# Optimization experiments

Hardware: AMD Instinct MI355X
Metric: run time of the kernel (lower is better)

## Reference

```python
import jax, jax.numpy as jnp
import numpy as np

DIVIDE = 1.0


def setup_inputs() -> dict:
    key = jax.random.key(0)
    ks = jax.random.split(key, 12)
    B, NH, L, H, DIM = 2, 8, 1024, 64, 64
    return {
        "mask": jax.random.normal(ks[0], (B, NH, L, L), dtype=jnp.float32),
        "q": jax.random.normal(ks[1], (B, L, NH, H), dtype=jnp.float32),
        "k": jax.random.normal(ks[2], (B, L, NH, H), dtype=jnp.float32),
        "v": jax.random.normal(ks[3], (B, L, NH, H), dtype=jnp.float32),
        "W0": jax.random.normal(ks[4], (1, DIM), dtype=jnp.float32) * 0.02,
        "b0": jnp.zeros((DIM,), dtype=jnp.float32),
        "W1": jax.random.normal(ks[5], (DIM, DIM), dtype=jnp.float32) * 0.02,
        "b1": jnp.zeros((DIM,), dtype=jnp.float32),
        "W2": jax.random.normal(ks[6], (DIM, DIM), dtype=jnp.float32) * 0.02,
        "b2": jnp.zeros((DIM,), dtype=jnp.float32),
        "Wf": jax.random.normal(ks[7], (DIM, 8), dtype=jnp.float32) * 0.02,
        "bf": jnp.zeros((8,), dtype=jnp.float32),
    }


def reference(mask, q, k, v, W0, b0, W1, b1, W2, b2, Wf, bf):
    # default positions: arange over L1 / L2; identical across batch so we
    # compute the (L1, L2) relative-position grid once and broadcast.
    L1, L2 = q.shape[-3], k.shape[-3]
    pos_q = jnp.arange(L1, dtype=q.dtype)
    pos_k = jnp.arange(L2, dtype=q.dtype)
    rel = (pos_q[:, None] - pos_k[None, :]) / DIVIDE          # (L1, L2)
    rel = rel[..., None]                                       # (L1, L2, 1)
    # depth-3 MLP: Linear -> SiLU (norm=False => Identity), final Linear to n_heads
    h = jax.nn.silu(rel @ W0 + b0)                             # (L1, L2, DIM)
    h = jax.nn.silu(h @ W1 + b1)
    h = jax.nn.silu(h @ W2 + b2)
    bias = h @ Wf + bf                                         # (L1, L2, NH)
    bias = jnp.moveaxis(bias, -1, 0)                           # (NH, L1, L2)
    # mask shapes already match q/k lengths -> no padding branch needed
    return mask - bias                                          # broadcast over B
```

## Files before the change

kernel.cpp:

```cpp
#include <hip/hip_runtime.h>
#include <hip/hip_bf16.h>


#define L_SEQ 1024
#define NDIAG (2 * L_SEQ - 1)
#define NH 8
#define DIM 64

typedef float f32x4 __attribute__((ext_vector_type(4)));

__device__ __forceinline__ float silu_f(float x) {
    return x / (1.0f + __expf(-x));
}

__global__ __launch_bounds__(256) void build_bias_table(
    const float* __restrict__ W0, const float* __restrict__ b0,
    const float* __restrict__ W1, const float* __restrict__ b1,
    const float* __restrict__ W2, const float* __restrict__ b2,
    const float* __restrict__ Wf, const float* __restrict__ bf,
    float* __restrict__ rtab ) {
    const int g = threadIdx.x >> 6;
    const int t = threadIdx.x & 63;
    const int d = blockIdx.x * 4 + g;
    const float rel = (float)(d - (L_SEQ - 1));

    __shared__ float sh[4][DIM];

    float h = silu_f(rel * W0[t] + b0[t]);
    sh[g][t] = h;
    __syncthreads();

    float acc = b1[t];
    #pragma unroll
    for (int k = 0; k < DIM; ++k) acc += sh[g][k] * W1[k * DIM + t];
    float h1 = silu_f(acc);
    __syncthreads();
    sh[g][t] = h1;
    __syncthreads();

    acc = b2[t];
    #pragma unroll
    for (int k = 0; k < DIM; ++k) acc += sh[g][k] * W2[k * DIM + t];
    float h2 = silu_f(acc);
    __syncthreads();
    sh[g][t] = h2;
    __syncthreads();

    if (t < NH && d < NDIAG) {
        float a = bf[t];
        #pragma unroll
        for (int k = 0; k < DIM; ++k) a += sh[g][k] * Wf[k * NH + t];
        rtab[t * NDIAG + (NDIAG - 1 - d)] = a;
    }
}

__global__ __launch_bounds__(256) void apply_bias(
    const f32x4* __restrict__ mask, const float* __restrict__ rtab,
    f32x4* __restrict__ out) {
    const int row = blockIdx.x;
    const int i = row & (L_SEQ - 1);
    const int h = (row >> 10) & (NH - 1);
    const float* rt = rtab + h * NDIAG + (L_SEQ - 1 - i);

    const int t = threadIdx.x;
    const int idx = row * 256 + t;
    const int j0 = t << 2;

    const f32x4 m = mask[idx];
    f32x4 o;
    o.x = m.x - rt[j0 + 0];
    o.y = m.y - rt[j0 + 1];
    o.z = m.z - rt[j0 + 2];
    o.w = m.w - rt[j0 + 3];
    out[idx] = o;
}

extern "C" void kernel_launch(void* const* d_in, const int* in_sizes, int n_in,
                              void* d_out, int out_size, void* d_ws, size_t ws_size,
                              hipStream_t stream) {
    const float* mask = (const float*)d_in[0];
    const float* W0 = (const float*)d_in[4];
    const float* b0 = (const float*)d_in[5];
    const float* W1 = (const float*)d_in[6];
    const float* b1 = (const float*)d_in[7];
    const float* W2 = (const float*)d_in[8];
    const float* b2 = (const float*)d_in[9];
    const float* Wf = (const float*)d_in[10];
    const float* bf = (const float*)d_in[11];
    float* out = (float*)d_out;

    float* rtab = (float*)d_ws;

    build_bias_table<<<(NDIAG + 3) / 4, 256, 0, stream>>>(
        W0, b0, W1, b1, W2, b2, Wf, bf, rtab);

    const int rows = out_size / L_SEQ;
    apply_bias<<<rows, 256, 0, stream>>>(
        (const f32x4*)mask, rtab, (f32x4*)out);
}
```

Baseline: 31.26 us.

## Stage bias diagonal window in LDS and reuse across rows and batches

Each apply_bias block now handles four query rows for one head across both batch elements. It first loads the shared 1027-entry diagonal window of the bias table into padded LDS, then reuses it for eight output rows. This removes the unaligned scalar global gathers of the table per row and cuts table traffic. The cost is more work per block, a sync, fewer blocks (2048), and a hardcoded B=2 grid.

```diff
diff --git a/kernel.cpp b/kernel.cpp
--- a/kernel.cpp
+++ b/kernel.cpp
@@ -54,25 +54,44 @@
     }
 }
 
+__device__ __forceinline__ int SW(int k) { return k + (k >> 5); }
+#define WIN 1027
+#define LDS_FLOATS (WIN + (WIN >> 5) + 1)
+
 __global__ __launch_bounds__(256) void apply_bias(
     const f32x4* __restrict__ mask, const float* __restrict__ rtab,
     f32x4* __restrict__ out) {
-    const int row = blockIdx.x;
-    const int i = row & (L_SEQ - 1);
-    const int h = (row >> 10) & (NH - 1);
-    const float* rt = rtab + h * NDIAG + (L_SEQ - 1 - i);
+    const int blk  = blockIdx.x;
+    const int h    = blk >> 8;
+    const int i0   = (blk & 255) << 2;
+    const int t    = threadIdx.x;
 
-    const int t = threadIdx.x;
-    const int idx = row * 256 + t;
-    const int j0 = t << 2;
+    __shared__ float w[LDS_FLOATS];
 
-    const f32x4 m = mask[idx];
-    f32x4 o;
-    o.x = m.x - rt[j0 + 0];
-    o.y = m.y - rt[j0 + 1];
-    o.z = m.z - rt[j0 + 2];
-    o.w = m.w - rt[j0 + 3];
-    out[idx] = o;
+    const float* src = rtab + h * NDIAG + (1020 - i0);
+    for (int k = t; k < WIN; k += 256) w[SW(k)] = src[k];
+    __syncthreads();
+
+    #pragma unroll
+    for (int r = 0; r < 4; ++r) {
+        const int off = (3 - r) + (t << 2);
+        const float v0 = w[SW(off + 0)];
+        const float v1 = w[SW(off + 1)];
+        const float v2 = w[SW(off + 2)];
+        const float v3 = w[SW(off + 3)];
+        const int i = i0 + r;
+        #pragma unroll
+        for (int b = 0; b < 2; ++b) {
+            const int idx = ((b * NH + h) * L_SEQ + i) * 256 + t;
+            const f32x4 m = mask[idx];
+            f32x4 o;
+            o.x = m.x - v0;
+            o.y = m.y - v1;
+            o.z = m.z - v2;
+            o.w = m.w - v3;
+            out[idx] = o;
+        }
+    }
 }
 
 extern "C" void kernel_launch(void* const* d_in, const int* in_sizes, int n_in,
@@ -94,7 +113,6 @@
     build_bias_table<<<(NDIAG + 3) / 4, 256, 0, stream>>>(
         W0, b0, W1, b1, W2, b2, Wf, bf, rtab);
 
-    const int rows = out_size / L_SEQ;
-    apply_bias<<<rows, 256, 0, stream>>>(
+    apply_bias<<<2048, 256, 0, stream>>>(
         (const f32x4*)mask, rtab, (f32x4*)out);
 }
```

New measurement: 32.17 us. +2.9%, slower.

## Fuse bias-table MLP and mask subtraction into one kernel with grid barrier

Applied to the files above, without the earlier changes.

Merges the two kernels into one 256-block launch. Each block first computes 8 diagonals of the relative-position MLP table, then waits on a global atomic counter before doing the subtraction pass. If the wait times out, the block recomputes the table entries it needs by itself. Each block then handles 64 rows with 1024 threads, reading the table through unaligned vector loads. This removes a kernel launch and the dependency gap between the two kernels, but adds a memset, a spin-wait barrier, and the risk of heavy fallback recomputation if not all blocks are resident at once.

```diff
diff --git a/kernel.cpp b/kernel.cpp
--- a/kernel.cpp
+++ b/kernel.cpp
@@ -8,77 +8,125 @@
 #define DIM 64
 
 typedef float f32x4 __attribute__((ext_vector_type(4)));
+typedef float f32x4u __attribute__((ext_vector_type(4), aligned(4)));
 
 __device__ __forceinline__ float silu_f(float x) {
     return x / (1.0f + __expf(-x));
 }
 
-__global__ __launch_bounds__(256) void build_bias_table(
+__device__ __forceinline__ void mlp_one(
+    int d, int tt, float* sh, bool act,
     const float* __restrict__ W0, const float* __restrict__ b0,
     const float* __restrict__ W1, const float* __restrict__ b1,
     const float* __restrict__ W2, const float* __restrict__ b2,
     const float* __restrict__ Wf, const float* __restrict__ bf,
-    float* __restrict__ rtab ) {
-    const int g = threadIdx.x >> 6;
-    const int t = threadIdx.x & 63;
-    const int d = blockIdx.x * 4 + g;
+    float* __restrict__ rtab) {
     const float rel = (float)(d - (L_SEQ - 1));
+    if (act) sh[tt] = silu_f(rel * W0[tt] + b0[tt]);
+    __syncthreads();
+    float a = 0.f;
+    if (act) {
+        a = b1[tt];
+        #pragma unroll
+        for (int k = 0; k < DIM; ++k) a += sh[k] * W1[k * DIM + tt];
+        a = silu_f(a);
+    }
+    __syncthreads();
+    if (act) sh[tt] = a;
+    __syncthreads();
+    if (act) {
+        a = b2[tt];
+        #pragma unroll
+        for (int k = 0; k < DIM; ++k) a += sh[k] * W2[k * DIM + tt];
+        a = silu_f(a);
+    }
+    __syncthreads();
+    if (act) sh[tt] = a;
+    __syncthreads();
+    if (act && tt < NH) {
+        float o = bf[tt];
+        #pragma unroll
+        for (int k = 0; k < DIM; ++k) o += sh[k] * Wf[k * NH + tt];
+        rtab[tt * NDIAG + (NDIAG - 1 - d)] = o;
+    }
+    __syncthreads();
+}
 
-    __shared__ float sh[4][DIM];
+__global__ __launch_bounds__(1024) void fused(
+    const f32x4* __restrict__ mask,
+    const float* __restrict__ W0, const float* __restrict__ b0,
+    const float* __restrict__ W1, const float* __restrict__ b1,
+    const float* __restrict__ W2, const float* __restrict__ b2,
+    const float* __restrict__ Wf, const float* __restrict__ bf,
+    float* __restrict__ rtab, unsigned int* __restrict__ cnt,
+    f32x4* __restrict__ out) {
+    const int blk = blockIdx.x;
+    const int t = threadIdx.x;
+    const int g = t >> 6;
+    const int tt = t & 63;
 
-    float h = silu_f(rel * W0[t] + b0[t]);
-    sh[g][t] = h;
+    __shared__ float sh[16][DIM];
+    __shared__ int ready;
+
+    {
+        const int d = blk * 8 + g;
+        const bool act = (g < 8) && (d < NDIAG);
+        mlp_one(d, tt, sh[g], act, W0, b0, W1, b1, W2, b2, Wf, bf, rtab);
+    }
+    if (t == 0) {
+        __hip_atomic_fetch_add(cnt, 1u, __ATOMIC_RELEASE,
+                               __HIP_MEMORY_SCOPE_AGENT);
+        int ok = 0;
+        for (int it = 0; it < 32768; ++it) {
+            if (__hip_atomic_load(cnt, __ATOMIC_ACQUIRE,
+                                  __HIP_MEMORY_SCOPE_AGENT) >= 256u) {
+                ok = 1; break;
+            }
+            __builtin_amdgcn_s_sleep(16);
+        }
+        ready = ok;
+    }
     __syncthreads();
 
-    float acc = b1[t];
-    #pragma unroll
-    for (int k = 0; k < DIM; ++k) acc += sh[g][k] * W1[k * DIM + t];
-    float h1 = silu_f(acc);
-    __syncthreads();
-    sh[g][t] = h1;
-    __syncthreads();
+    const int b_ = blk >> 7;
+    const int h = (blk >> 4) & 7;
+    const int i0 = (blk & 15) << 6;
 
-    acc = b2[t];
-    #pragma unroll
-    for (int k = 0; k < DIM; ++k) acc += sh[g][k] * W2[k * DIM + t];
-    float h2 = silu_f(acc);
-    __syncthreads();
-    sh[g][t] = h2;
-    __syncthreads();
+    if (!ready) {
+        for (int p = 0; p < 68; ++p) {
+            const int d = i0 + p * 16 + g;
+            const bool act = (d <= i0 + 1086) && (d < NDIAG);
+            mlp_one(d, tt, sh[g], act, W0, b0, W1, b1, W2, b2, Wf, bf, rtab);
+        }
+    }
 
-    if (t < NH && d < NDIAG) {
-        float a = bf[t];
-        #pragma unroll
-        for (int k = 0; k < DIM; ++k) a += sh[g][k] * Wf[k * NH + t];
-        rtab[t * NDIAG + (NDIAG - 1 - d)] = a;
+    const int tc = t & 255;
+    const int g4 = t >> 8;
+    const int j0 = tc << 2;
+    const float* rth = rtab + h * NDIAG + (L_SEQ - 1);
+    const long rowbase = (long)((b_ * NH + h) * L_SEQ + i0) * 256;
+    const f32x4* mrow = mask + rowbase;
+    f32x4* orow = out + rowbase;
+
+    #pragma unroll 4
+    for (int k = 0; k < 16; ++k) {
+        const int r = g4 + (k << 2);
+        const int i = i0 + r;
+        const f32x4u v = *(const f32x4u*)(rth - i + j0);
+        const f32x4 m = mrow[r * 256 + tc];
+        f32x4 o;
+        o.x = m.x - v.x;
+        o.y = m.y - v.y;
+        o.z = m.z - v.z;
+        o.w = m.w - v.w;
+        orow[r * 256 + tc] = o;
     }
-}
-
-__global__ __launch_bounds__(256) void apply_bias(
-    const f32x4* __restrict__ mask, const float* __restrict__ rtab,
-    f32x4* __restrict__ out) {
-    const int row = blockIdx.x;
-    const int i = row & (L_SEQ - 1);
-    const int h = (row >> 10) & (NH - 1);
-    const float* rt = rtab + h * NDIAG + (L_SEQ - 1 - i);
-
-    const int t = threadIdx.x;
-    const int idx = row * 256 + t;
-    const int j0 = t << 2;
-
-    const f32x4 m = mask[idx];
-    f32x4 o;
-    o.x = m.x - rt[j0 + 0];
-    o.y = m.y - rt[j0 + 1];
-    o.z = m.z - rt[j0 + 2];
-    o.w = m.w - rt[j0 + 3];
-    out[idx] = o;
 }
 
 extern "C" void kernel_launch(void* const* d_in, const int* in_sizes, int n_in,
                               void* d_out, int out_size, void* d_ws, size_t ws_size,
                               hipStream_t stream) {
-    const float* mask = (const float*)d_in[0];
+    const f32x4* mask = (const f32x4*)d_in[0];
     const float* W0 = (const float*)d_in[4];
     const float* b0 = (const float*)d_in[5];
     const float* W1 = (const float*)d_in[6];
@@ -87,14 +135,12 @@
     const float* b2 = (const float*)d_in[9];
     const float* Wf = (const float*)d_in[10];
     const float* bf = (const float*)d_in[11];
-    float* out = (float*)d_out;
+    f32x4* out = (f32x4*)d_out;
 
     float* rtab = (float*)d_ws;
+    unsigned int* cnt = (unsigned int*)((char*)d_ws + 65504);
 
-    build_bias_table<<<(NDIAG + 3) / 4, 256, 0, stream>>>(
-        W0, b0, W1, b1, W2, b2, Wf, bf, rtab);
-
-    const int rows = out_size / L_SEQ;
-    apply_bias<<<rows, 256, 0, stream>>>(
-        (const f32x4*)mask, rtab, (f32x4*)out);
+    hipMemsetAsync(cnt, 0, sizeof(unsigned int), stream);
+    fused<<<256, 1024, 0, stream>>>(mask, W0, b0, W1, b1, W2, b2, Wf, bf,
+                                    rtab, cnt, out);
 }
```

New measurement: 48.44 us. 55.0% more time.
